# Optimization experiments

Hardware: AMD Instinct MI355X
Metric: run time of the kernel (lower is better)

Reference implementation:

```python
import jax, jax.numpy as jnp
import numpy as np

B, T, C = 4, 1024, 1024
H, D = 16, 64  # num_heads, head_channels
EPS = 1e-5


def layernorm(x, g, b):
    mu = jnp.mean(x, axis=-1, keepdims=True)
    d = x - mu
    var = jnp.mean(d * d, axis=-1, keepdims=True)
    return d * jax.lax.rsqrt(var + EPS) * g + b


def setup_inputs() -> dict:
    key = jax.random.key(0)
    ks = jax.random.split(key, 5)
    s = 0.02  # init scale for weights
    return {
        "x": jax.random.normal(ks[0], (B, T, C), jnp.float32),
        "norm_g": jnp.ones((C,), jnp.float32),
        "norm_b": jnp.zeros((C,), jnp.float32),
        "qkv_w": jax.random.normal(ks[1], (C, 3 * C), jnp.float32) * s,
        "qkv_b": jax.random.normal(ks[2], (3 * C,), jnp.float32) * s,
        "qln_g": jnp.ones((C,), jnp.float32),
        "qln_b": jnp.zeros((C,), jnp.float32),
        "kln_g": jnp.ones((C,), jnp.float32),
        "kln_b": jnp.zeros((C,), jnp.float32),
        "proj_w": jax.random.normal(ks[3], (C, C), jnp.float32) * s,
        "proj_b": jax.random.normal(ks[4], (C,), jnp.float32) * s,
    }


def reference(x, norm_g, norm_b, qkv_w, qkv_b, qln_g, qln_b, kln_g, kln_b, proj_w, proj_b):
    in_dtype = x.dtype
    # pre-LN computed in fp32, cast back to input dtype
    xn = layernorm(x.astype(jnp.float32), norm_g, norm_b).astype(in_dtype)
    qkv = xn @ qkv_w + qkv_b  # [B,T,3C]
    q, k, v = jnp.split(qkv, 3, axis=-1)
    # per-Q/K LayerNorm over the full channel dim (before head split)
    q = layernorm(q, qln_g, qln_b)
    k = layernorm(k, kln_g, kln_b)
    # [B,T,C] -> [B,H,T,D]
    to_heads = lambda t: t.reshape(B, T, H, D).transpose(0, 2, 1, 3)
    q, k, v = to_heads(q), to_heads(k), to_heads(v)
    temp = 1.0
    scale = (D ** -0.5) / temp  # sqrt_scale**2 / temp
    scores = jnp.einsum("bhqd,bhkd->bhqk", q, k) * scale
    attn = jax.nn.softmax(scores, axis=-1)
    out = jnp.einsum("bhqk,bhkd->bhqd", attn, v)
    out = out.transpose(0, 2, 1, 3).reshape(B, T, C)
    return out @ proj_w + proj_b
```

## Files before the change

kernel.cpp:

```cpp
#include <hip/hip_runtime.h>
#include <math.h>

#define T_SEQ 1024
#define C_DIM 1024
#define NB    4
#define NH    16
#define HD    64
#define C3    3072

typedef __attribute__((ext_vector_type(8))) short bf16x8;
typedef __attribute__((ext_vector_type(4))) float f32x4;
typedef unsigned short u16;

union B8 { bf16x8 v; u16 u[8]; unsigned d[4]; };

__device__ inline u16 bf16_rtn(float v) {
    unsigned int u = __float_as_uint(v);
    u += 0x7FFFu + ((u >> 16) & 1u);
    return (u16)(u >> 16);
}
__device__ inline void split_bf16(float v, u16& hi, u16& lo) {
    hi = bf16_rtn(v);
    float hif = __uint_as_float(((unsigned int)hi) << 16);
    lo = bf16_rtn(v - hif);
}

__global__ __launch_bounds__(256) void ln_split_kernel(const float* __restrict__ in,
                                                       u16* __restrict__ oh,
                                                       u16* __restrict__ ol,
                                                       const float* __restrict__ g,
                                                       const float* __restrict__ beta) {
    const int row = blockIdx.x;
    const float* x = in + (size_t)row * 1024;
    const int t = threadIdx.x;

    float4 v = *(const float4*)&x[t * 4];
    float s  = v.x + v.y + v.z + v.w;
    float ss = v.x * v.x + v.y * v.y + v.z * v.z + v.w * v.w;
    #pragma unroll
    for (int m = 1; m < 64; m <<= 1) {
        s  += __shfl_xor(s, m);
        ss += __shfl_xor(ss, m);
    }
    __shared__ float red[8];
    const int wave = t >> 6, lane = t & 63;
    if (lane == 0) { red[wave * 2] = s; red[wave * 2 + 1] = ss; }
    __syncthreads();
    s  = red[0] + red[2] + red[4] + red[6];
    ss = red[1] + red[3] + red[5] + red[7];

    const float mu   = s * (1.0f / 1024.0f);
    const float var  = ss * (1.0f / 1024.0f) - mu * mu;
    const float rstd = rsqrtf(var + 1e-5f);

    float4 gg = *(const float4*)&g[t * 4];
    float4 bb = *(const float4*)&beta[t * 4];
    float o[4];
    o[0] = (v.x - mu) * rstd * gg.x + bb.x;
    o[1] = (v.y - mu) * rstd * gg.y + bb.y;
    o[2] = (v.z - mu) * rstd * gg.z + bb.z;
    o[3] = (v.w - mu) * rstd * gg.w + bb.w;

    ushort4 h4, l4;
    split_bf16(o[0], h4.x, l4.x);
    split_bf16(o[1], h4.y, l4.y);
    split_bf16(o[2], h4.z, l4.z);
    split_bf16(o[3], h4.w, l4.w);
    size_t off = (size_t)row * 1024 + t * 4;
    *(ushort4*)&oh[off] = h4;
    *(ushort4*)&ol[off] = l4;
}

__global__ __launch_bounds__(256) void ln_qk_kernel(float* __restrict__ qkv,
                                                    const float* __restrict__ qg,
                                                    const float* __restrict__ qb,
                                                    const float* __restrict__ kg,
                                                    const float* __restrict__ kb) {
    const int row = blockIdx.x;
    const int isK = row >> 12;
    const int r = row & 4095;
    float* x = qkv + (size_t)r * C3 + (isK ? 1024 : 0);
    const float* g    = isK ? kg : qg;
    const float* beta = isK ? kb : qb;
    const int t = threadIdx.x;

    float4 v = *(const float4*)&x[t * 4];
    float s  = v.x + v.y + v.z + v.w;
    float ss = v.x * v.x + v.y * v.y + v.z * v.z + v.w * v.w;
    #pragma unroll
    for (int m = 1; m < 64; m <<= 1) {
        s  += __shfl_xor(s, m);
        ss += __shfl_xor(ss, m);
    }
    __shared__ float red[8];
    const int wave = t >> 6, lane = t & 63;
    if (lane == 0) { red[wave * 2] = s; red[wave * 2 + 1] = ss; }
    __syncthreads();
    s  = red[0] + red[2] + red[4] + red[6];
    ss = red[1] + red[3] + red[5] + red[7];

    const float mu   = s * (1.0f / 1024.0f);
    const float var  = ss * (1.0f / 1024.0f) - mu * mu;
    const float rstd = rsqrtf(var + 1e-5f);

    float4 gg = *(const float4*)&g[t * 4];
    float4 bb = *(const float4*)&beta[t * 4];
    float4 o;
    o.x = (v.x - mu) * rstd * gg.x + bb.x;
    o.y = (v.y - mu) * rstd * gg.y + bb.y;
    o.z = (v.z - mu) * rstd * gg.z + bb.z;
    o.w = (v.w - mu) * rstd * gg.w + bb.w;
    *(float4*)&x[t * 4] = o;
}

__global__ __launch_bounds__(256) void wsplit_t(const float* __restrict__ W,
                                                u16* __restrict__ Th,
                                                u16* __restrict__ Tl,
                                                int K, int N) {
    __shared__ float tile[64][69];
    const int n0 = blockIdx.x * 64, k0 = blockIdx.y * 64;
    const int t = threadIdx.x;
    #pragma unroll
    for (int i = 0; i < 4; ++i) {
        int idx = t + 256 * i;
        int kr = idx >> 4, nc = (idx & 15) * 4;
        float4 v = *(const float4*)&W[(size_t)(k0 + kr) * N + n0 + nc];
        tile[kr][nc + 0] = v.x; tile[kr][nc + 1] = v.y;
        tile[kr][nc + 2] = v.z; tile[kr][nc + 3] = v.w;
    }
    __syncthreads();
    #pragma unroll
    for (int i = 0; i < 4; ++i) {
        int idx = t + 256 * i;
        int nr = idx >> 4, kc = (idx & 15) * 4;
        ushort4 h4, l4;
        split_bf16(tile[kc + 0][nr], h4.x, l4.x);
        split_bf16(tile[kc + 1][nr], h4.y, l4.y);
        split_bf16(tile[kc + 2][nr], h4.z, l4.z);
        split_bf16(tile[kc + 3][nr], h4.w, l4.w);
        size_t o = (size_t)(n0 + nr) * K + k0 + kc;
        *(ushort4*)&Th[o] = h4;
        *(ushort4*)&Tl[o] = l4;
    }
}

__global__ __launch_bounds__(256) void gemm_mfma_split(
    const u16* __restrict__ Ah, const u16* __restrict__ Al,
    const u16* __restrict__ Bh, const u16* __restrict__ Bl,
    const float* __restrict__ bias, float* __restrict__ C,
    int M, int N, int K) {
    __shared__ u16 sAh[128 * 32], sAl[128 * 32], sBh[128 * 32], sBl[128 * 32];

    const int t    = threadIdx.x;
    const int lane = t & 63;
    const int wid  = t >> 6;
    const int wr   = wid >> 1, wc = wid & 1;

    const int nbx = gridDim.x;
    const int nwg = nbx * gridDim.y;
    int bid = blockIdx.y * nbx + blockIdx.x;
    int swz = (bid & 7) * (nwg >> 3) + (bid >> 3);
    const int bn = (swz % nbx) * 128;
    const int bm = (swz / nbx) * 128;

    const int jr    = lane >> 2;
    const int cphys = lane & 3;
    const int m16 = lane & 15, g8 = lane >> 4;

    f32x4 acc[4][4];
    #pragma unroll
    for (int m = 0; m < 4; ++m)
        #pragma unroll
        for (int n = 0; n < 4; ++n) {
            f32x4 z = {0.0f, 0.0f, 0.0f, 0.0f};
            acc[m][n] = z;
        }

    for (int k0 = 0; k0 < K; k0 += 32) {
        __syncthreads();
        #pragma unroll
        for (int jj = 0; jj < 2; ++jj) {
            const int j = wid * 2 + jj;
            const int r = (j << 4) + jr;
            const int cl = cphys ^ (r & 3);
            const size_t ga = ((size_t)(bm + r) * K + k0 + (cl << 3)) * 2;
            const size_t gb = ((size_t)(bn + r) * K + k0 + (cl << 3)) * 2;
            const unsigned ldso = (unsigned)(j << 10);
            __builtin_amdgcn_global_load_lds(
                (const __attribute__((address_space(1))) void*)((const char*)Ah + ga),
                (__attribute__((address_space(3))) void*)((char*)sAh + ldso), 16, 0, 0);
            __builtin_amdgcn_global_load_lds(
                (const __attribute__((address_space(1))) void*)((const char*)Al + ga),
                (__attribute__((address_space(3))) void*)((char*)sAl + ldso), 16, 0, 0);
            __builtin_amdgcn_global_load_lds(
                (const __attribute__((address_space(1))) void*)((const char*)Bh + gb),
                (__attribute__((address_space(3))) void*)((char*)sBh + ldso), 16, 0, 0);
            __builtin_amdgcn_global_load_lds(
                (const __attribute__((address_space(1))) void*)((const char*)Bl + gb),
                (__attribute__((address_space(3))) void*)((char*)sBl + ldso), 16, 0, 0);
        }
        __syncthreads();

        bf16x8 ah[4], al[4], bh[4], bl[4];
        #pragma unroll
        for (int m = 0; m < 4; ++m) {
            const int r = wr * 64 + m * 16 + m16;
            const int off = (r << 5) + ((g8 ^ (m16 & 3)) << 3);
            ah[m] = *(const bf16x8*)&sAh[off];
            al[m] = *(const bf16x8*)&sAl[off];
        }
        #pragma unroll
        for (int n = 0; n < 4; ++n) {
            const int r = wc * 64 + n * 16 + m16;
            const int off = (r << 5) + ((g8 ^ (m16 & 3)) << 3);
            bh[n] = *(const bf16x8*)&sBh[off];
            bl[n] = *(const bf16x8*)&sBl[off];
        }
        #pragma unroll
        for (int m = 0; m < 4; ++m)
            #pragma unroll
            for (int n = 0; n < 4; ++n) {
                acc[m][n] = __builtin_amdgcn_mfma_f32_16x16x32_bf16(ah[m], bh[n], acc[m][n], 0, 0, 0);
                acc[m][n] = __builtin_amdgcn_mfma_f32_16x16x32_bf16(al[m], bh[n], acc[m][n], 0, 0, 0);
                acc[m][n] = __builtin_amdgcn_mfma_f32_16x16x32_bf16(ah[m], bl[n], acc[m][n], 0, 0, 0);
            }
    }

    #pragma unroll
    for (int m = 0; m < 4; ++m) {
        const int row0 = bm + wr * 64 + m * 16 + (g8 << 2);
        #pragma unroll
        for (int n = 0; n < 4; ++n) {
            const int col = bn + wc * 64 + n * 16 + m16;
            const float bv = bias[col];
            #pragma unroll
            for (int e = 0; e < 4; ++e)
                C[(size_t)(row0 + e) * N + col] = acc[m][n][e] + bv;
        }
    }
}

__global__ __launch_bounds__(256) void attn_mfma(const float* __restrict__ qkv,
                                                 u16* __restrict__ att_hi,
                                                 u16* __restrict__ att_lo) {
    __shared__ __align__(16) u16 SM[24576];
    u16* Kh = SM;
    u16* Kl = SM + 4096;
    u16* Vh = SM + 8192;
    u16* Vl = SM + 12288;
    u16* Ph = SM + 16384;
    u16* Pl = SM + 20480;

    const int t    = threadIdx.x;
    const int lane = t & 63;
    const int wv   = t >> 6;
    const int m16  = lane & 15, g8 = lane >> 4;

    const int bid  = blockIdx.x;
    const int work = (bid & 7) * 128 + (bid >> 3);
    const int qt = work & 15;
    const int bh = work >> 4;
    const int h  = bh & 15;
    const int b  = bh >> 4;
    const int q0 = qt * 64;

    const float* qp = qkv + (size_t)b * T_SEQ * C3 + h * HD;
    const float* kp = qp + 1024;
    const float* vp = qp + 2048;

    bf16x8 qh[2], ql[2];
    {
        const float* qrow = qp + (size_t)(q0 + wv * 16 + m16) * C3;
        #pragma unroll
        for (int ds = 0; ds < 2; ++ds) {
            float4 a = *(const float4*)&qrow[ds * 32 + g8 * 8];
            float4 c = *(const float4*)&qrow[ds * 32 + g8 * 8 + 4];
            float q8[8] = {a.x, a.y, a.z, a.w, c.x, c.y, c.z, c.w};
            B8 hh, ll;
            #pragma unroll
            for (int j = 0; j < 8; ++j) {
                float v = q8[j] * 0.125f;
                u16 hi, lo;
                split_bf16(v, hi, lo);
                hh.u[j] = hi; ll.u[j] = lo;
            }
            qh[ds] = hh.v; ql[ds] = ll.v;
        }
    }

    float kreg[16], vreg[16];

    auto load_tile = [&](int kt) {
        const int kb = kt * 64;
        #pragma unroll
        for (int i = 0; i < 2; ++i) {
            int c = t + 256 * i;
            int kr = c >> 3, dg8 = c & 7;
            float4 a = *(const float4*)&kp[(size_t)(kb + kr) * C3 + dg8 * 8];
            float4 d = *(const float4*)&kp[(size_t)(kb + kr) * C3 + dg8 * 8 + 4];
            kreg[i * 8 + 0] = a.x; kreg[i * 8 + 1] = a.y;
            kreg[i * 8 + 2] = a.z; kreg[i * 8 + 3] = a.w;
            kreg[i * 8 + 4] = d.x; kreg[i * 8 + 5] = d.y;
            kreg[i * 8 + 6] = d.z; kreg[i * 8 + 7] = d.w;
        }
        #pragma unroll
        for (int i = 0; i < 16; ++i)
            vreg[i] = vp[(size_t)(kb + wv * 16 + i) * C3 + lane];
    };

    auto write_tile = [&]() {
        #pragma unroll
        for (int i = 0; i < 2; ++i) {
            int c = t + 256 * i;
            int kr = c >> 3, dg8 = c & 7;
            B8 hh, ll;
            #pragma unroll
            for (int j = 0; j < 8; ++j) split_bf16(kreg[i * 8 + j], hh.u[j], ll.u[j]);
            int idx = kr * 64 + ((dg8 ^ (kr & 7)) << 3);
            *(bf16x8*)&Kh[idx] = hh.v;
            *(bf16x8*)&Kl[idx] = ll.v;
        }
        B8 vh0, vl0, vh1, vl1;
        #pragma unroll
        for (int i = 0; i < 8; ++i)  split_bf16(vreg[i],     vh0.u[i], vl0.u[i]);
        #pragma unroll
        for (int i = 0; i < 8; ++i)  split_bf16(vreg[i + 8], vh1.u[i], vl1.u[i]);
        const int vb = lane * 64;
        *(bf16x8*)&Vh[vb + (((wv * 2 + 0) ^ (lane & 7)) << 3)] = vh0.v;
        *(bf16x8*)&Vh[vb + (((wv * 2 + 1) ^ (lane & 7)) << 3)] = vh1.v;
        *(bf16x8*)&Vl[vb + (((wv * 2 + 0) ^ (lane & 7)) << 3)] = vl0.v;
        *(bf16x8*)&Vl[vb + (((wv * 2 + 1) ^ (lane & 7)) << 3)] = vl1.v;
    };

    f32x4 acc_o[4];
    #pragma unroll
    for (int i = 0; i < 4; ++i) { f32x4 z = {0,0,0,0}; acc_o[i] = z; }
    float m_run = -INFINITY, l_run = 0.0f;

    u16* Phw = Ph + wv * 1024;
    u16* Plw = Pl + wv * 1024;

    load_tile(0);
    write_tile();
    __syncthreads();

    for (int kt = 0; kt < 16; ++kt) {
        if (kt < 15) load_tile(kt + 1);

        f32x4 accs[4];
        #pragma unroll
        for (int i = 0; i < 4; ++i) { f32x4 z = {0,0,0,0}; accs[i] = z; }
        #pragma unroll
        for (int ds = 0; ds < 2; ++ds) {
            #pragma unroll
            for (int sub = 0; sub < 4; ++sub) {
                const int row = sub * 16 + m16;
                const int idx = row * 64 + (((ds * 4 + g8) ^ (m16 & 7)) << 3);
                bf16x8 kh = *(const bf16x8*)&Kh[idx];
                bf16x8 kl = *(const bf16x8*)&Kl[idx];
                accs[sub] = __builtin_amdgcn_mfma_f32_16x16x32_bf16(kh, qh[ds], accs[sub], 0, 0, 0);
                accs[sub] = __builtin_amdgcn_mfma_f32_16x16x32_bf16(kl, qh[ds], accs[sub], 0, 0, 0);
                accs[sub] = __builtin_amdgcn_mfma_f32_16x16x32_bf16(kh, ql[ds], accs[sub], 0, 0, 0);
            }
        }

        float mt = accs[0][0];
        #pragma unroll
        for (int sub = 0; sub < 4; ++sub)
            #pragma unroll
            for (int e = 0; e < 4; ++e) mt = fmaxf(mt, accs[sub][e]);
        mt = fmaxf(mt, __shfl_xor(mt, 16));
        mt = fmaxf(mt, __shfl_xor(mt, 32));
        const float mnew = fmaxf(m_run, mt);
        const float fsc = __expf(m_run - mnew);
        float p[4][4];
        float ts = 0.0f;
        #pragma unroll
        for (int sub = 0; sub < 4; ++sub)
            #pragma unroll
            for (int e = 0; e < 4; ++e) {
                p[sub][e] = __expf(accs[sub][e] - mnew);
                ts += p[sub][e];
            }
        ts += __shfl_xor(ts, 16);
        ts += __shfl_xor(ts, 32);
        l_run = l_run * fsc + ts;
        m_run = mnew;
        #pragma unroll
        for (int d = 0; d < 4; ++d)
            #pragma unroll
            for (int e = 0; e < 4; ++e) acc_o[d][e] *= fsc;

        #pragma unroll
        for (int sub = 0; sub < 4; ++sub)
            #pragma unroll
            for (int pp = 0; pp < 2; ++pp) {
                float p0 = p[sub][2 * pp], p1 = p[sub][2 * pp + 1];
                u16 h0, l0, h1, l1;
                split_bf16(p0, h0, l0);
                split_bf16(p1, h1, l1);
                unsigned hw = (unsigned)h0 | ((unsigned)h1 << 16);
                unsigned lw = (unsigned)l0 | ((unsigned)l1 << 16);
                const int idx = m16 * 64 + (((2 * sub + (g8 >> 1)) ^ (m16 & 7)) << 3)
                                + 4 * (g8 & 1) + 2 * pp;
                *(unsigned*)&Phw[idx] = hw;
                *(unsigned*)&Plw[idx] = lw;
            }

        bf16x8 pfh[2], pfl[2];
        #pragma unroll
        for (int ks = 0; ks < 2; ++ks) {
            const int idx = m16 * 64 + (((ks * 4 + g8) ^ (m16 & 7)) << 3);
            pfh[ks] = *(const bf16x8*)&Phw[idx];
            pfl[ks] = *(const bf16x8*)&Plw[idx];
        }

        #pragma unroll
        for (int dsub = 0; dsub < 4; ++dsub) {
            #pragma unroll
            for (int ks = 0; ks < 2; ++ks) {
                const int vrow = dsub * 16 + m16;
                const int vidx = vrow * 64 + (((ks * 4 + g8) ^ (m16 & 7)) << 3);
                bf16x8 vh = *(const bf16x8*)&Vh[vidx];
                bf16x8 vl = *(const bf16x8*)&Vl[vidx];
                acc_o[dsub] = __builtin_amdgcn_mfma_f32_16x16x32_bf16(vh, pfh[ks], acc_o[dsub], 0, 0, 0);
                acc_o[dsub] = __builtin_amdgcn_mfma_f32_16x16x32_bf16(vh, pfl[ks], acc_o[dsub], 0, 0, 0);
                acc_o[dsub] = __builtin_amdgcn_mfma_f32_16x16x32_bf16(vl, pfh[ks], acc_o[dsub], 0, 0, 0);
            }
        }

        __syncthreads();
        if (kt < 15) { write_tile(); __syncthreads(); }
    }

    const float linv = 1.0f / l_run;
    #pragma unroll
    for (int dsub = 0; dsub < 4; ++dsub)
        #pragma unroll
        for (int pp = 0; pp < 2; ++pp) {
            float o0 = acc_o[dsub][2 * pp] * linv;
            float o1 = acc_o[dsub][2 * pp + 1] * linv;
            u16 h0, l0, h1, l1;
            split_bf16(o0, h0, l0);
            split_bf16(o1, h1, l1);
            unsigned hw = (unsigned)h0 | ((unsigned)h1 << 16);
            unsigned lw = (unsigned)l0 | ((unsigned)l1 << 16);
            const int idx = m16 * 64 + (((2 * dsub + (g8 >> 1)) ^ (m16 & 7)) << 3)
                            + 4 * (g8 & 1) + 2 * pp;
            *(unsigned*)&Phw[idx] = hw;
            *(unsigned*)&Plw[idx] = lw;
        }
    __syncthreads();
    #pragma unroll
    for (int i = 0; i < 2; ++i) {
        int s = t + 256 * i;
        int q_l = s >> 3, dg8 = s & 7;
        const int idx = q_l * 64 + ((dg8 ^ (q_l & 7)) << 3);
        bf16x8 oh = *(const bf16x8*)&Ph[idx];
        bf16x8 ol = *(const bf16x8*)&Pl[idx];
        size_t off = (size_t)(b * T_SEQ + q0 + q_l) * C_DIM + h * HD + dg8 * 8;
        *(bf16x8*)&att_hi[off] = oh;
        *(bf16x8*)&att_lo[off] = ol;
    }
}

extern "C" void kernel_launch(void* const* d_in, const int* in_sizes, int n_in,
                              void* d_out, int out_size, void* d_ws, size_t ws_size,
                              hipStream_t stream) {
    const float* x      = (const float*)d_in[0];
    const float* norm_g = (const float*)d_in[1];
    const float* norm_b = (const float*)d_in[2];
    const float* qkv_w  = (const float*)d_in[3];
    const float* qkv_b  = (const float*)d_in[4];
    const float* qln_g  = (const float*)d_in[5];
    const float* qln_b  = (const float*)d_in[6];
    const float* kln_g  = (const float*)d_in[7];
    const float* kln_b  = (const float*)d_in[8];
    const float* proj_w = (const float*)d_in[9];
    const float* proj_b = (const float*)d_in[10];
    float* out = (float*)d_out;

    char* w = (char*)d_ws;
    float* qkv  = (float*)w;
    u16* xn_hi  = (u16*)(w + 50331648);
    u16* xn_lo  = (u16*)(w + 58720256);
    u16* wq_hi  = (u16*)(w + 67108864);
    u16* wq_lo  = (u16*)(w + 73400320);
    u16* pw_hi  = (u16*)(w + 79691776);
    u16* pw_lo  = (u16*)(w + 81788928);
    u16* att_hi = xn_hi;
    u16* att_lo = xn_lo;

    const int rows = NB * T_SEQ;

    ln_split_kernel<<<rows, 256, 0, stream>>>(x, xn_hi, xn_lo, norm_g, norm_b);
    wsplit_t<<<dim3(C3 / 64, C_DIM / 64), 256, 0, stream>>>(qkv_w, wq_hi, wq_lo, C_DIM, C3);
    wsplit_t<<<dim3(C_DIM / 64, C_DIM / 64), 256, 0, stream>>>(proj_w, pw_hi, pw_lo, C_DIM, C_DIM);
    gemm_mfma_split<<<dim3(C3 / 128, rows / 128), 256, 0, stream>>>(
        xn_hi, xn_lo, wq_hi, wq_lo, qkv_b, qkv, rows, C3, C_DIM);
    ln_qk_kernel<<<2 * rows, 256, 0, stream>>>(qkv, qln_g, qln_b, kln_g, kln_b);
    attn_mfma<<<NB * NH * (T_SEQ / 64), 256, 0, stream>>>(qkv, att_hi, att_lo);
    gemm_mfma_split<<<dim3(C_DIM / 128, rows / 128), 256, 0, stream>>>(
        att_hi, att_lo, pw_hi, pw_lo, proj_b, out, rows, C_DIM, C_DIM);
}
```

Before: 342.5 us.

## Pre-split K/V to bf16 head-major layouts and stream them via direct-to-LDS loads

The K half of the QK LayerNorm now writes bf16 hi/lo pairs in a per-head contiguous layout. A new kernel transposes and splits V the same way. The attention kernel then stages K and V tiles with global_load_lds, double-buffers V and uses raw barriers, replacing per-block fp32 loads and in-kernel splitting. Workspace is reused aggressively: the attention output and the proj weights are packed inside the qkv buffer using leading-dimension strides. This removes redundant conversion work across the 16 query tiles per head, at the cost of an extra kernel and tighter buffer-aliasing assumptions.

```diff
diff --git a/kernel.cpp b/kernel.cpp
--- a/kernel.cpp
+++ b/kernel.cpp
@@ -75,7 +75,9 @@
                                                     const float* __restrict__ qg,
                                                     const float* __restrict__ qb,
                                                     const float* __restrict__ kg,
-                                                    const float* __restrict__ kb) {
+                                                    const float* __restrict__ kb,
+                                                    u16* __restrict__ Kh,
+                                                    u16* __restrict__ Kl) {
     const int row = blockIdx.x;
     const int isK = row >> 12;
     const int r = row & 4095;
@@ -105,18 +107,65 @@
 
     float4 gg = *(const float4*)&g[t * 4];
     float4 bb = *(const float4*)&beta[t * 4];
-    float4 o;
-    o.x = (v.x - mu) * rstd * gg.x + bb.x;
-    o.y = (v.y - mu) * rstd * gg.y + bb.y;
-    o.z = (v.z - mu) * rstd * gg.z + bb.z;
-    o.w = (v.w - mu) * rstd * gg.w + bb.w;
-    *(float4*)&x[t * 4] = o;
+    float o0 = (v.x - mu) * rstd * gg.x + bb.x;
+    float o1 = (v.y - mu) * rstd * gg.y + bb.y;
+    float o2 = (v.z - mu) * rstd * gg.z + bb.z;
+    float o3 = (v.w - mu) * rstd * gg.w + bb.w;
+
+    if (!isK) {
+        float4 o = {o0, o1, o2, o3};
+        *(float4*)&x[t * 4] = o;
+    } else {
+        ushort4 h4, l4;
+        split_bf16(o0, h4.x, l4.x);
+        split_bf16(o1, h4.y, l4.y);
+        split_bf16(o2, h4.z, l4.z);
+        split_bf16(o3, h4.w, l4.w);
+        const int c = t * 4;
+        const int hh = c >> 6, d = c & 63;
+        const int b = r >> 10, tt = r & 1023;
+        size_t off = ((size_t)((b << 4) + hh) << 16) + (size_t)tt * 64 + d;
+        *(ushort4*)&Kh[off] = h4;
+        *(ushort4*)&Kl[off] = l4;
+    }
+}
+
+__global__ __launch_bounds__(256) void vsplit_t(const float* __restrict__ qkv,
+                                                u16* __restrict__ Vth,
+                                                u16* __restrict__ Vtl) {
+    __shared__ float tile[64][68];
+    const int bid = blockIdx.x;
+    const int tt = bid & 15, h = (bid >> 4) & 15, b = bid >> 8;
+    const int t = threadIdx.x;
+    const float* src = qkv + (size_t)(b * 1024 + tt * 64) * C3 + 2048 + h * 64;
+    #pragma unroll
+    for (int i = 0; i < 4; ++i) {
+        int idx = i * 256 + t;
+        int tr = idx >> 4, dc = (idx & 15) * 4;
+        float4 v = *(const float4*)&src[(size_t)tr * C3 + dc];
+        tile[tr][dc + 0] = v.x; tile[tr][dc + 1] = v.y;
+        tile[tr][dc + 2] = v.z; tile[tr][dc + 3] = v.w;
+    }
+    __syncthreads();
+    #pragma unroll
+    for (int i = 0; i < 4; ++i) {
+        int idx = i * 256 + t;
+        int d = idx >> 4, tc = (idx & 15) * 4;
+        ushort4 h4, l4;
+        split_bf16(tile[tc + 0][d], h4.x, l4.x);
+        split_bf16(tile[tc + 1][d], h4.y, l4.y);
+        split_bf16(tile[tc + 2][d], h4.z, l4.z);
+        split_bf16(tile[tc + 3][d], h4.w, l4.w);
+        size_t off = ((size_t)((b * 16 + h) * 64 + d)) * 1024 + tt * 64 + tc;
+        *(ushort4*)&Vth[off] = h4;
+        *(ushort4*)&Vtl[off] = l4;
+    }
 }
 
 __global__ __launch_bounds__(256) void wsplit_t(const float* __restrict__ W,
                                                 u16* __restrict__ Th,
                                                 u16* __restrict__ Tl,
-                                                int K, int N) {
+                                                int K, int N, int ldt) {
     __shared__ float tile[64][69];
     const int n0 = blockIdx.x * 64, k0 = blockIdx.y * 64;
     const int t = threadIdx.x;
@@ -138,7 +187,7 @@
         split_bf16(tile[kc + 1][nr], h4.y, l4.y);
         split_bf16(tile[kc + 2][nr], h4.z, l4.z);
         split_bf16(tile[kc + 3][nr], h4.w, l4.w);
-        size_t o = (size_t)(n0 + nr) * K + k0 + kc;
+        size_t o = (size_t)(n0 + nr) * ldt + k0 + kc;
         *(ushort4*)&Th[o] = h4;
         *(ushort4*)&Tl[o] = l4;
     }
@@ -148,7 +197,7 @@
     const u16* __restrict__ Ah, const u16* __restrict__ Al,
     const u16* __restrict__ Bh, const u16* __restrict__ Bl,
     const float* __restrict__ bias, float* __restrict__ C,
-    int M, int N, int K) {
+    int M, int N, int K, int lda, int ldb) {
     __shared__ u16 sAh[128 * 32], sAl[128 * 32], sBh[128 * 32], sBl[128 * 32];
 
     const int t    = threadIdx.x;
@@ -183,8 +232,8 @@
             const int j = wid * 2 + jj;
             const int r = (j << 4) + jr;
             const int cl = cphys ^ (r & 3);
-            const size_t ga = ((size_t)(bm + r) * K + k0 + (cl << 3)) * 2;
-            const size_t gb = ((size_t)(bn + r) * K + k0 + (cl << 3)) * 2;
+            const size_t ga = ((size_t)(bm + r) * lda + k0 + (cl << 3)) * 2;
+            const size_t gb = ((size_t)(bn + r) * ldb + k0 + (cl << 3)) * 2;
             const unsigned ldso = (unsigned)(j << 10);
             __builtin_amdgcn_global_load_lds(
                 (const __attribute__((address_space(1))) void*)((const char*)Ah + ga),
@@ -241,15 +290,12 @@
 }
 
 __global__ __launch_bounds__(256) void attn_mfma(const float* __restrict__ qkv,
-                                                 u16* __restrict__ att_hi,
-                                                 u16* __restrict__ att_lo) {
-    __shared__ __align__(16) u16 SM[24576];
-    u16* Kh = SM;
-    u16* Kl = SM + 4096;
-    u16* Vh = SM + 8192;
-    u16* Vl = SM + 12288;
-    u16* Ph = SM + 16384;
-    u16* Pl = SM + 20480;
+                                                 const u16* __restrict__ Kh,
+                                                 const u16* __restrict__ Kl,
+                                                 const u16* __restrict__ Vth,
+                                                 const u16* __restrict__ Vtl,
+                                                 u16* __restrict__ att) {
+    __shared__ __align__(16) u16 SM[32768];
 
     const int t    = threadIdx.x;
     const int lane = t & 63;
@@ -264,13 +310,44 @@
     const int b  = bh >> 4;
     const int q0 = qt * 64;
 
-    const float* qp = qkv + (size_t)b * T_SEQ * C3 + h * HD;
-    const float* kp = qp + 1024;
-    const float* vp = qp + 2048;
+    const int srow = lane >> 3;
+    const int scl  = (lane & 7) ^ srow;
+    const size_t kvrow0 = (size_t)bh << 16;
+
+    auto stageK = [&](int kt) {
+        const int kb = kt * 64;
+        #pragma unroll
+        for (int issue = 0; issue < 2; ++issue) {
+            const int rloc = (issue * 4 + wv) * 8 + srow;
+            const size_t go = (kvrow0 + (size_t)(kb + rloc) * 64 + scl * 8) * 2;
+            const unsigned lo = (unsigned)((issue * 4 + wv) * 1024);
+            __builtin_amdgcn_global_load_lds(
+                (const __attribute__((address_space(1))) void*)((const char*)Kh + go),
+                (__attribute__((address_space(3))) void*)((char*)SM + lo), 16, 0, 0);
+            __builtin_amdgcn_global_load_lds(
+                (const __attribute__((address_space(1))) void*)((const char*)Kl + go),
+                (__attribute__((address_space(3))) void*)((char*)SM + 8192 + lo), 16, 0, 0);
+        }
+    };
+    auto stageV = [&](int kt, int bsel) {
+        const int kb = kt * 64;
+        #pragma unroll
+        for (int issue = 0; issue < 2; ++issue) {
+            const int rloc = (issue * 4 + wv) * 8 + srow;
+            const size_t go = (kvrow0 + (size_t)rloc * 1024 + kb + scl * 8) * 2;
+            const unsigned lo = (unsigned)(16384 + bsel * 16384 + (issue * 4 + wv) * 1024);
+            __builtin_amdgcn_global_load_lds(
+                (const __attribute__((address_space(1))) void*)((const char*)Vth + go),
+                (__attribute__((address_space(3))) void*)((char*)SM + lo), 16, 0, 0);
+            __builtin_amdgcn_global_load_lds(
+                (const __attribute__((address_space(1))) void*)((const char*)Vtl + go),
+                (__attribute__((address_space(3))) void*)((char*)SM + 8192 + lo), 16, 0, 0);
+        }
+    };
 
     bf16x8 qh[2], ql[2];
     {
-        const float* qrow = qp + (size_t)(q0 + wv * 16 + m16) * C3;
+        const float* qrow = qkv + (size_t)(b * T_SEQ + q0 + wv * 16 + m16) * C3 + h * HD;
         #pragma unroll
         for (int ds = 0; ds < 2; ++ds) {
             float4 a = *(const float4*)&qrow[ds * 32 + g8 * 8];
@@ -279,90 +356,51 @@
             B8 hh, ll;
             #pragma unroll
             for (int j = 0; j < 8; ++j) {
-                float v = q8[j] * 0.125f;
                 u16 hi, lo;
-                split_bf16(v, hi, lo);
+                split_bf16(q8[j] * 0.125f, hi, lo);
                 hh.u[j] = hi; ll.u[j] = lo;
             }
             qh[ds] = hh.v; ql[ds] = ll.v;
         }
     }
 
-    float kreg[16], vreg[16];
-
-    auto load_tile = [&](int kt) {
-        const int kb = kt * 64;
-        #pragma unroll
-        for (int i = 0; i < 2; ++i) {
-            int c = t + 256 * i;
-            int kr = c >> 3, dg8 = c & 7;
-            float4 a = *(const float4*)&kp[(size_t)(kb + kr) * C3 + dg8 * 8];
-            float4 d = *(const float4*)&kp[(size_t)(kb + kr) * C3 + dg8 * 8 + 4];
-            kreg[i * 8 + 0] = a.x; kreg[i * 8 + 1] = a.y;
-            kreg[i * 8 + 2] = a.z; kreg[i * 8 + 3] = a.w;
-            kreg[i * 8 + 4] = d.x; kreg[i * 8 + 5] = d.y;
-            kreg[i * 8 + 6] = d.z; kreg[i * 8 + 7] = d.w;
-        }
-        #pragma unroll
-        for (int i = 0; i < 16; ++i)
-            vreg[i] = vp[(size_t)(kb + wv * 16 + i) * C3 + lane];
-    };
-
-    auto write_tile = [&]() {
-        #pragma unroll
-        for (int i = 0; i < 2; ++i) {
-            int c = t + 256 * i;
-            int kr = c >> 3, dg8 = c & 7;
-            B8 hh, ll;
-            #pragma unroll
-            for (int j = 0; j < 8; ++j) split_bf16(kreg[i * 8 + j], hh.u[j], ll.u[j]);
-            int idx = kr * 64 + ((dg8 ^ (kr & 7)) << 3);
-            *(bf16x8*)&Kh[idx] = hh.v;
-            *(bf16x8*)&Kl[idx] = ll.v;
-        }
-        B8 vh0, vl0, vh1, vl1;
-        #pragma unroll
-        for (int i = 0; i < 8; ++i)  split_bf16(vreg[i],     vh0.u[i], vl0.u[i]);
-        #pragma unroll
-        for (int i = 0; i < 8; ++i)  split_bf16(vreg[i + 8], vh1.u[i], vl1.u[i]);
-        const int vb = lane * 64;
-        *(bf16x8*)&Vh[vb + (((wv * 2 + 0) ^ (lane & 7)) << 3)] = vh0.v;
-        *(bf16x8*)&Vh[vb + (((wv * 2 + 1) ^ (lane & 7)) << 3)] = vh1.v;
-        *(bf16x8*)&Vl[vb + (((wv * 2 + 0) ^ (lane & 7)) << 3)] = vl0.v;
-        *(bf16x8*)&Vl[vb + (((wv * 2 + 1) ^ (lane & 7)) << 3)] = vl1.v;
-    };
-
     f32x4 acc_o[4];
     #pragma unroll
-    for (int i = 0; i < 4; ++i) { f32x4 z = {0,0,0,0}; acc_o[i] = z; }
+    for (int i = 0; i < 4; ++i) { f32x4 z = {0, 0, 0, 0}; acc_o[i] = z; }
     float m_run = -INFINITY, l_run = 0.0f;
 
-    u16* Phw = Ph + wv * 1024;
-    u16* Plw = Pl + wv * 1024;
-
-    load_tile(0);
-    write_tile();
-    __syncthreads();
-
+    u16* Phw = SM + 24576 + wv * 1024;
+    u16* Plw = SM + 28672 + wv * 1024;
+
+    stageK(0);
+    stageV(0, 0);
+    asm volatile("s_waitcnt vmcnt(0)" ::: "memory");
+    __builtin_amdgcn_s_barrier();
+    __builtin_amdgcn_sched_barrier(0);
+
+    int vsel = 0;
     for (int kt = 0; kt < 16; ++kt) {
-        if (kt < 15) load_tile(kt + 1);
-
         f32x4 accs[4];
         #pragma unroll
-        for (int i = 0; i < 4; ++i) { f32x4 z = {0,0,0,0}; accs[i] = z; }
+        for (int i = 0; i < 4; ++i) { f32x4 z = {0, 0, 0, 0}; accs[i] = z; }
         #pragma unroll
         for (int ds = 0; ds < 2; ++ds) {
             #pragma unroll
             for (int sub = 0; sub < 4; ++sub) {
                 const int row = sub * 16 + m16;
-                const int idx = row * 64 + (((ds * 4 + g8) ^ (m16 & 7)) << 3);
-                bf16x8 kh = *(const bf16x8*)&Kh[idx];
-                bf16x8 kl = *(const bf16x8*)&Kl[idx];
+                const int idx = row * 64 + ((((ds * 4 + g8)) ^ (m16 & 7)) << 3);
+                bf16x8 kh = *(const bf16x8*)&SM[idx];
+                bf16x8 kl = *(const bf16x8*)&SM[4096 + idx];
                 accs[sub] = __builtin_amdgcn_mfma_f32_16x16x32_bf16(kh, qh[ds], accs[sub], 0, 0, 0);
                 accs[sub] = __builtin_amdgcn_mfma_f32_16x16x32_bf16(kl, qh[ds], accs[sub], 0, 0, 0);
                 accs[sub] = __builtin_amdgcn_mfma_f32_16x16x32_bf16(kh, ql[ds], accs[sub], 0, 0, 0);
             }
         }
+
+        __builtin_amdgcn_sched_barrier(0);
+        __builtin_amdgcn_s_barrier();
+        __builtin_amdgcn_sched_barrier(0);
+        if (kt < 15) { stageK(kt + 1); stageV(kt + 1, vsel ^ 1); }
 
         float mt = accs[0][0];
         #pragma unroll
@@ -410,27 +448,31 @@
         bf16x8 pfh[2], pfl[2];
         #pragma unroll
         for (int ks = 0; ks < 2; ++ks) {
-            const int idx = m16 * 64 + (((ks * 4 + g8) ^ (m16 & 7)) << 3);
+            const int idx = m16 * 64 + ((((ks * 4 + g8)) ^ (m16 & 7)) << 3);
             pfh[ks] = *(const bf16x8*)&Phw[idx];
             pfl[ks] = *(const bf16x8*)&Plw[idx];
         }
 
+        const int vb = 8192 + vsel * 8192;
         #pragma unroll
         for (int dsub = 0; dsub < 4; ++dsub) {
             #pragma unroll
             for (int ks = 0; ks < 2; ++ks) {
                 const int vrow = dsub * 16 + m16;
-                const int vidx = vrow * 64 + (((ks * 4 + g8) ^ (m16 & 7)) << 3);
-                bf16x8 vh = *(const bf16x8*)&Vh[vidx];
-                bf16x8 vl = *(const bf16x8*)&Vl[vidx];
+                const int vidx = vb + vrow * 64 + ((((ks * 4 + g8)) ^ (m16 & 7)) << 3);
+                bf16x8 vh = *(const bf16x8*)&SM[vidx];
+                bf16x8 vl = *(const bf16x8*)&SM[4096 + vidx];
                 acc_o[dsub] = __builtin_amdgcn_mfma_f32_16x16x32_bf16(vh, pfh[ks], acc_o[dsub], 0, 0, 0);
                 acc_o[dsub] = __builtin_amdgcn_mfma_f32_16x16x32_bf16(vh, pfl[ks], acc_o[dsub], 0, 0, 0);
                 acc_o[dsub] = __builtin_amdgcn_mfma_f32_16x16x32_bf16(vl, pfh[ks], acc_o[dsub], 0, 0, 0);
             }
         }
 
-        __syncthreads();
-        if (kt < 15) { write_tile(); __syncthreads(); }
+        __builtin_amdgcn_sched_barrier(0);
+        asm volatile("s_waitcnt vmcnt(0)" ::: "memory");
+        __builtin_amdgcn_s_barrier();
+        __builtin_amdgcn_sched_barrier(0);
+        vsel ^= 1;
     }
 
     const float linv = 1.0f / l_run;
@@ -456,11 +498,11 @@
         int s = t + 256 * i;
         int q_l = s >> 3, dg8 = s & 7;
         const int idx = q_l * 64 + ((dg8 ^ (q_l & 7)) << 3);
-        bf16x8 oh = *(const bf16x8*)&Ph[idx];
-        bf16x8 ol = *(const bf16x8*)&Pl[idx];
-        size_t off = (size_t)(b * T_SEQ + q0 + q_l) * C_DIM + h * HD + dg8 * 8;
-        *(bf16x8*)&att_hi[off] = oh;
-        *(bf16x8*)&att_lo[off] = ol;
+        bf16x8 oh = *(const bf16x8*)&SM[24576 + idx];
+        bf16x8 ol = *(const bf16x8*)&SM[28672 + idx];
+        size_t off = (size_t)(b * T_SEQ + q0 + q_l) * 6144 + 2048 + h * HD + dg8 * 8;
+        *(bf16x8*)&att[off] = oh;
+        *(bf16x8*)&att[off + 1024] = ol;
     }
 }
 
@@ -481,25 +523,31 @@
     float* out = (float*)d_out;
 
     char* w = (char*)d_ws;
-    float* qkv  = (float*)w;
-    u16* xn_hi  = (u16*)(w + 50331648);
-    u16* xn_lo  = (u16*)(w + 58720256);
-    u16* wq_hi  = (u16*)(w + 67108864);
-    u16* wq_lo  = (u16*)(w + 73400320);
-    u16* pw_hi  = (u16*)(w + 79691776);
-    u16* pw_lo  = (u16*)(w + 81788928);
-    u16* att_hi = xn_hi;
-    u16* att_lo = xn_lo;
+    float* qkv    = (float*)w;
+    u16* qkv_u16  = (u16*)w;
+    u16* xn_hi    = (u16*)(w + 50331648);
+    u16* xn_lo    = (u16*)(w + 58720256);
+    u16* wq_hi    = (u16*)(w + 67108864);
+    u16* wq_lo    = (u16*)(w + 73400320);
+    u16* Kh       = xn_hi;
+    u16* Kl       = xn_lo;
+    u16* Vth      = (u16*)(w + 67108864);
+    u16* Vtl      = (u16*)(w + 75497472);
+    u16* pw_hi    = qkv_u16 + 4096;
+    u16* pw_lo    = qkv_u16 + 5120;
+    u16* att_hi   = qkv_u16 + 2048;
+    u16* att_lo   = qkv_u16 + 3072;
 
     const int rows = NB * T_SEQ;
 
     ln_split_kernel<<<rows, 256, 0, stream>>>(x, xn_hi, xn_lo, norm_g, norm_b);
-    wsplit_t<<<dim3(C3 / 64, C_DIM / 64), 256, 0, stream>>>(qkv_w, wq_hi, wq_lo, C_DIM, C3);
-    wsplit_t<<<dim3(C_DIM / 64, C_DIM / 64), 256, 0, stream>>>(proj_w, pw_hi, pw_lo, C_DIM, C_DIM);
+    wsplit_t<<<dim3(C3 / 64, C_DIM / 64), 256, 0, stream>>>(qkv_w, wq_hi, wq_lo, C_DIM, C3, 1024);
     gemm_mfma_split<<<dim3(C3 / 128, rows / 128), 256, 0, stream>>>(
-        xn_hi, xn_lo, wq_hi, wq_lo, qkv_b, qkv, rows, C3, C_DIM);
-    ln_qk_kernel<<<2 * rows, 256, 0, stream>>>(qkv, qln_g, qln_b, kln_g, kln_b);
-    attn_mfma<<<NB * NH * (T_SEQ / 64), 256, 0, stream>>>(qkv, att_hi, att_lo);
+        xn_hi, xn_lo, wq_hi, wq_lo, qkv_b, qkv, rows, C3, C_DIM, 1024, 1024);
+    ln_qk_kernel<<<2 * rows, 256, 0, stream>>>(qkv, qln_g, qln_b, kln_g, kln_b, Kh, Kl);
+    vsplit_t<<<1024, 256, 0, stream>>>(qkv, Vth, Vtl);
+    wsplit_t<<<dim3(C_DIM / 64, C_DIM / 64), 256, 0, stream>>>(proj_w, pw_hi, pw_lo, C_DIM, C_DIM, 6144);
+    attn_mfma<<<1024, 256, 0, stream>>>(qkv, Kh, Kl, Vth, Vtl, qkv_u16);
     gemm_mfma_split<<<dim3(C_DIM / 128, rows / 128), 256, 0, stream>>>(
-        att_hi, att_lo, pw_hi, pw_lo, proj_b, out, rows, C_DIM, C_DIM);
-}
+        att_hi, att_lo, pw_hi, pw_lo, proj_b, out, rows, C_DIM, C_DIM, 6144, 6144);
+}
```

Measured after the change: 337.3 us. No clear change (-1.5%).
